# Performance work log

Measured on AMD Instinct MI355X. Metric: run time of the kernel, lower is better.

Reference implementation:

```python
import jax, jax.numpy as jnp
import numpy as np

INPUT_SIZE = 512
HIDDEN_SIZE = 512


def setup_inputs() -> dict:
    key = jax.random.key(0)
    k1, k2, k3, k4, k5 = jax.random.split(key, 5)
    B, N = 8, 2048
    x = jax.random.normal(k1, (B, N, INPUT_SIZE), dtype=jnp.float32)
    # Linear params (torch nn.Linear: y = x @ W^T + b), init scale ~ 1/sqrt(fan_in)
    s = 1.0 / np.sqrt(INPUT_SIZE)
    Wq = jax.random.uniform(k2, (HIDDEN_SIZE, INPUT_SIZE), minval=-s, maxval=s, dtype=jnp.float32)
    bq = jax.random.uniform(k3, (HIDDEN_SIZE,), minval=-s, maxval=s, dtype=jnp.float32)
    Wk = jax.random.uniform(k4, (HIDDEN_SIZE, INPUT_SIZE), minval=-s, maxval=s, dtype=jnp.float32)
    bk = jax.random.uniform(k5, (HIDDEN_SIZE,), minval=-s, maxval=s, dtype=jnp.float32)
    return {"x": x, "Wq": Wq, "bq": bq, "Wk": Wk, "bk": bk}


def reference(x, Wq, bq, Wk, bk):
    # q, k: [B, N, H]
    q = jnp.einsum('bnd,hd->bnh', x, Wq) + bq
    k = jnp.einsum('bnd,hd->bnh', x, Wk) + bk
    # scores: [B, N, N], softmax over last axis (dim=2)
    scores = jnp.einsum('bnh,bmh->bnm', q, k) / jnp.sqrt(jnp.float32(HIDDEN_SIZE))
    attn = jax.nn.softmax(scores, axis=2)
    # attended = attn^T @ x : [B, N, input_size]; squeeze(2) no-op since input_size>1
    attended = jnp.einsum('bnm,bnd->bmd', attn, x)
    return attended
```

## Files before the change

kernel.cpp:

```cpp
#include <hip/hip_runtime.h>

typedef __bf16 bf16x8 __attribute__((ext_vector_type(8)));
typedef float f32x4 __attribute__((ext_vector_type(4)));

__device__ __forceinline__ ushort f2bf(float f) {
    union { float f; unsigned u; } v; v.f = f;
    unsigned r = v.u + 0x7FFF + ((v.u >> 16) & 1);
    return (ushort)(r >> 16);
}

__device__ __forceinline__ void async_copy16(const void* g, void* l) {
    __builtin_amdgcn_global_load_lds(
        (const __attribute__((address_space(1))) void*)g,
        (__attribute__((address_space(3))) void*)l, 16, 0, 0);
}

__global__ __launch_bounds__(256) void cvt_kernel(
    const float4* __restrict__ x, const float4* __restrict__ Wq,
    const float4* __restrict__ Wk, const float4* __restrict__ bq,
    const float4* __restrict__ bk,
    ushort4* __restrict__ xb, ushort4* __restrict__ Wb,
    float4* __restrict__ biasc) {
    int i = blockIdx.x * 256 + threadIdx.x;
    if (i < 2097152) {
        float4 v = x[i];
        ushort4 r; r.x = f2bf(v.x); r.y = f2bf(v.y); r.z = f2bf(v.z); r.w = f2bf(v.w);
        xb[i] = r;
    }
    if (i < 131072) {
        float4 v = (i < 65536) ? Wq[i] : Wk[i - 65536];
        ushort4 r; r.x = f2bf(v.x); r.y = f2bf(v.y); r.z = f2bf(v.z); r.w = f2bf(v.w);
        Wb[i] = r;
    }
    if (i < 256) {
        biasc[i] = (i < 128) ? bq[i] : bk[i - 128];
    }
}

__global__ __launch_bounds__(256) void fold_kernel(
    const float* __restrict__ x, const float* __restrict__ Z,
    ushort* __restrict__ xzT) {
    __shared__ float tile[64][65];
    __shared__ float zin[64];
    const int b = blockIdx.y;
    const int td = blockIdx.x & 7;
    const int tn = blockIdx.x >> 3;
    const int n0 = tn * 64, d0 = td * 64;
    const int t = threadIdx.x;
    if (t < 64) zin[t] = 1.0f / Z[b * 2048 + n0 + t];
    __syncthreads();
    const int c = t & 63, r0 = t >> 6;
#pragma unroll
    for (int j = 0; j < 16; ++j) {
        int r = r0 + j * 4;
        tile[r][c] = x[((size_t)b * 2048 + n0 + r) * 512 + d0 + c] * zin[r];
    }
    __syncthreads();
#pragma unroll
    for (int j = 0; j < 16; ++j) {
        int dr = r0 + j * 4;
        xzT[((size_t)b * 512 + d0 + dr) * 2048 + n0 + c] = f2bf(tile[c][dr]);
    }
}

template <int EPI>
__global__ __launch_bounds__(256) void gemm_bt(
    const ushort* __restrict__ A, int lda, long sA,
    const ushort* __restrict__ B, int ldb, long sB,
    void* __restrict__ C, int ldc, long sC,
    int M, int N, int K,
    const float* __restrict__ bias, float scale,
    float* __restrict__ Z, long sZ) {
    __shared__ ushort lA[128 * 64];
    __shared__ ushort lB[128 * 64];
    const int b = blockIdx.y;
    A += (size_t)b * sA;
    B += (size_t)b * sB;
    const int tiles_n = N >> 7;
    const int tm = blockIdx.x / tiles_n, tn = blockIdx.x % tiles_n;
    const int t = threadIdx.x;
    const int l = t & 63, w = t >> 6;
    const int wr = w >> 1, wc = w & 1;

    f32x4 acc[4][4];
#pragma unroll
    for (int i = 0; i < 4; ++i)
#pragma unroll
        for (int j = 0; j < 4; ++j) acc[i][j] = (f32x4){0.f, 0.f, 0.f, 0.f};

    for (int k0 = 0; k0 < K; k0 += 64) {
#pragma unroll
        for (int p = 0; p < 4; ++p) {
            int off = p * 4096 + t * 16;
            int row = off >> 7;
            int kb = off & 127;
            int kswz = kb ^ ((row & 7) << 4);
            const ushort* srcA = A + (size_t)(tm * 128 + row) * lda + k0 + (kswz >> 1);
            async_copy16(srcA, (char*)lA + off);
            const ushort* srcB = B + (size_t)(tn * 128 + row) * ldb + k0 + (kswz >> 1);
            async_copy16(srcB, (char*)lB + off);
        }
        __syncthreads();
#pragma unroll
        for (int ks = 0; ks < 2; ++ks) {
            bf16x8 af[4], bfr[4];
#pragma unroll
            for (int i = 0; i < 4; ++i) {
                int row = wr * 64 + i * 16 + (l & 15);
                int colb = (ks * 64 + (l >> 4) * 16) ^ ((row & 7) << 4);
                af[i] = *(const bf16x8*)((const char*)lA + row * 128 + colb);
            }
#pragma unroll
            for (int j = 0; j < 4; ++j) {
                int row = wc * 64 + j * 16 + (l & 15);
                int colb = (ks * 64 + (l >> 4) * 16) ^ ((row & 7) << 4);
                bfr[j] = *(const bf16x8*)((const char*)lB + row * 128 + colb);
            }
#pragma unroll
            for (int i = 0; i < 4; ++i)
#pragma unroll
                for (int j = 0; j < 4; ++j)
                    acc[i][j] = __builtin_amdgcn_mfma_f32_16x16x32_bf16(
                        af[i], bfr[j], acc[i][j], 0, 0, 0);
        }
        __syncthreads();
    }

    const int m_base = tm * 128 + wr * 64;
    const int n_base = tn * 128 + wc * 64;

    if (EPI == 0) {
        ushort* Cp = (ushort*)C + (size_t)b * sC;
#pragma unroll
        for (int i = 0; i < 4; ++i)
#pragma unroll
            for (int j = 0; j < 4; ++j)
#pragma unroll
                for (int q = 0; q < 4; ++q) {
                    int row = m_base + i * 16 + (l >> 4) * 4 + q;
                    int col = n_base + j * 16 + (l & 15);
                    Cp[(size_t)row * ldc + col] = f2bf(acc[i][j][q] + bias[col]);
                }
    } else if (EPI == 1) {
        ushort* Cp = (ushort*)C + (size_t)b * sC;
        float colsum[4] = {0.f, 0.f, 0.f, 0.f};
#pragma unroll
        for (int i = 0; i < 4; ++i)
#pragma unroll
            for (int j = 0; j < 4; ++j)
#pragma unroll
                for (int q = 0; q < 4; ++q) {
                    int row = m_base + i * 16 + (l >> 4) * 4 + q;
                    int col = n_base + j * 16 + (l & 15);
                    float e = __expf(acc[i][j][q] * scale);
                    Cp[(size_t)row * ldc + col] = f2bf(e);
                    colsum[j] += e;
                }
#pragma unroll
        for (int j = 0; j < 4; ++j) {
            float s = colsum[j];
            s += __shfl_xor(s, 16);
            s += __shfl_xor(s, 32);
            if (l < 16) atomicAdd(&Z[b * sZ + n_base + j * 16 + l], s);
        }
    } else {
        float* Cp = (float*)C + (size_t)b * sC;
#pragma unroll
        for (int i = 0; i < 4; ++i)
#pragma unroll
            for (int j = 0; j < 4; ++j)
#pragma unroll
                for (int q = 0; q < 4; ++q) {
                    int row = m_base + i * 16 + (l >> 4) * 4 + q;
                    int col = n_base + j * 16 + (l & 15);
                    Cp[(size_t)row * ldc + col] = acc[i][j][q];
                }
    }
}

extern "C" void kernel_launch(void* const* d_in, const int* in_sizes, int n_in,
                              void* d_out, int out_size, void* d_ws, size_t ws_size,
                              hipStream_t stream) {
    const float* x  = (const float*)d_in[0];
    const float* Wq = (const float*)d_in[1];
    const float* bq = (const float*)d_in[2];
    const float* Wk = (const float*)d_in[3];
    const float* bk = (const float*)d_in[4];

    char* ws = (char*)d_ws;
    ushort* xb    = (ushort*)(ws);
    ushort* Wb    = (ushort*)(ws + 16777216);
    float*  biasc = (float*) (ws + 17825792);
    float*  Z     = (float*) (ws + 17829888);
    ushort* qkb   = (ushort*)(ws + 17895424);
    ushort* E     = (ushort*)(ws + 51449856);
    ushort* xzT   = xb;

    hipMemsetAsync(Z, 0, 16384 * 4, stream);

    cvt_kernel<<<8192, 256, 0, stream>>>(
        (const float4*)x, (const float4*)Wq, (const float4*)Wk,
        (const float4*)bq, (const float4*)bk,
        (ushort4*)xb, (ushort4*)Wb, (float4*)biasc);

    gemm_bt<0><<<dim3(1024, 1), 256, 0, stream>>>(
        xb, 512, 0L, Wb, 512, 0L, qkb, 1024, 0L,
        16384, 1024, 512, biasc, 0.f, nullptr, 0L);

    gemm_bt<1><<<dim3(256, 8), 256, 0, stream>>>(
        qkb + 512, 1024, 2048L * 1024, qkb, 1024, 2048L * 1024,
        E, 2048, 2048L * 2048, 2048, 2048, 512,
        nullptr, 0.04419417382415922f, Z, 2048L);

    fold_kernel<<<dim3(256, 8), 256, 0, stream>>>(x, Z, xzT);

    gemm_bt<2><<<dim3(64, 8), 256, 0, stream>>>(
        E, 2048, 2048L * 2048, xzT, 2048, 512L * 2048,
        d_out, 512, 2048L * 512, 2048, 512, 2048,
        nullptr, 0.f, nullptr, 0L);
}
```

Baseline: 154.4 us.

## Vectorize bf16 epilogue stores with column permutation and fold from bf16 input

The GEMM epilogues now pack four accumulator columns into one 8-byte bf16 store instead of scattered 2-byte stores. This permutes columns within each 64-wide block, and the code keeps that consistent: the Z atomics, the fold kernel's normalizer indexing and the q/k hidden dimension all follow the same permutation. The fold kernel reads the bf16 copy of x with vector loads instead of the fp32 original and writes packed bf16x4, which cuts its memory traffic. Manual rounding is replaced by native __bf16 conversions. The permuted layout is subtle and fragile, but the indexing appears consistent.

```diff
diff --git a/kernel.cpp b/kernel.cpp
--- a/kernel.cpp
+++ b/kernel.cpp
@@ -1,13 +1,8 @@
 #include <hip/hip_runtime.h>
 
 typedef __bf16 bf16x8 __attribute__((ext_vector_type(8)));
+typedef __bf16 bf16x4 __attribute__((ext_vector_type(4)));
 typedef float f32x4 __attribute__((ext_vector_type(4)));
-
-__device__ __forceinline__ ushort f2bf(float f) {
-    union { float f; unsigned u; } v; v.f = f;
-    unsigned r = v.u + 0x7FFF + ((v.u >> 16) & 1);
-    return (ushort)(r >> 16);
-}
 
 __device__ __forceinline__ void async_copy16(const void* g, void* l) {
     __builtin_amdgcn_global_load_lds(
@@ -19,17 +14,17 @@
     const float4* __restrict__ x, const float4* __restrict__ Wq,
     const float4* __restrict__ Wk, const float4* __restrict__ bq,
     const float4* __restrict__ bk,
-    ushort4* __restrict__ xb, ushort4* __restrict__ Wb,
+    bf16x4* __restrict__ xb, bf16x4* __restrict__ Wb,
     float4* __restrict__ biasc) {
     int i = blockIdx.x * 256 + threadIdx.x;
     if (i < 2097152) {
         float4 v = x[i];
-        ushort4 r; r.x = f2bf(v.x); r.y = f2bf(v.y); r.z = f2bf(v.z); r.w = f2bf(v.w);
+        bf16x4 r = {(__bf16)v.x, (__bf16)v.y, (__bf16)v.z, (__bf16)v.w};
         xb[i] = r;
     }
     if (i < 131072) {
         float4 v = (i < 65536) ? Wq[i] : Wk[i - 65536];
-        ushort4 r; r.x = f2bf(v.x); r.y = f2bf(v.y); r.z = f2bf(v.z); r.w = f2bf(v.w);
+        bf16x4 r = {(__bf16)v.x, (__bf16)v.y, (__bf16)v.z, (__bf16)v.w};
         Wb[i] = r;
     }
     if (i < 256) {
@@ -38,7 +33,7 @@
 }
 
 __global__ __launch_bounds__(256) void fold_kernel(
-    const float* __restrict__ x, const float* __restrict__ Z,
+    const __bf16* __restrict__ xb, const float* __restrict__ Z,
     ushort* __restrict__ xzT) {
     __shared__ float tile[64][65];
     __shared__ float zin[64];
@@ -49,17 +44,25 @@
     const int t = threadIdx.x;
     if (t < 64) zin[t] = 1.0f / Z[b * 2048 + n0 + t];
     __syncthreads();
-    const int c = t & 63, r0 = t >> 6;
-#pragma unroll
-    for (int j = 0; j < 16; ++j) {
-        int r = r0 + j * 4;
-        tile[r][c] = x[((size_t)b * 2048 + n0 + r) * 512 + d0 + c] * zin[r];
+    const int cl = t & 15, c4 = cl * 4, rr = t >> 4;
+#pragma unroll
+    for (int j = 0; j < 4; ++j) {
+        int nr = rr + j * 16;
+        bf16x4 v = *(const bf16x4*)&xb[((size_t)b * 2048 + n0 + nr) * 512 + d0 + c4];
+        tile[nr][c4 + 0] = (float)v[0];
+        tile[nr][c4 + 1] = (float)v[1];
+        tile[nr][c4 + 2] = (float)v[2];
+        tile[nr][c4 + 3] = (float)v[3];
     }
     __syncthreads();
 #pragma unroll
-    for (int j = 0; j < 16; ++j) {
-        int dr = r0 + j * 4;
-        xzT[((size_t)b * 512 + d0 + dr) * 2048 + n0 + c] = f2bf(tile[c][dr]);
+    for (int j2 = 0; j2 < 4; ++j2) {
+        int dr = rr + j2 * 16;
+        bf16x4 pk;
+#pragma unroll
+        for (int j = 0; j < 4; ++j)
+            pk[j] = (__bf16)(tile[j * 16 + cl][dr] * zin[c4 + j]);
+        *(bf16x4*)&xzT[((size_t)b * 512 + d0 + dr) * 2048 + n0 + c4] = pk;
     }
 }
 
@@ -68,7 +71,7 @@
     const ushort* __restrict__ A, int lda, long sA,
     const ushort* __restrict__ B, int ldb, long sB,
     void* __restrict__ C, int ldc, long sC,
-    int M, int N, int K,
+    int tiles_n, int K,
     const float* __restrict__ bias, float scale,
     float* __restrict__ Z, long sZ) {
     __shared__ ushort lA[128 * 64];
@@ -76,7 +79,6 @@
     const int b = blockIdx.y;
     A += (size_t)b * sA;
     B += (size_t)b * sB;
-    const int tiles_n = N >> 7;
     const int tm = blockIdx.x / tiles_n, tn = blockIdx.x % tiles_n;
     const int t = threadIdx.x;
     const int l = t & 63, w = t >> 6;
@@ -95,10 +97,10 @@
             int row = off >> 7;
             int kb = off & 127;
             int kswz = kb ^ ((row & 7) << 4);
-            const ushort* srcA = A + (size_t)(tm * 128 + row) * lda + k0 + (kswz >> 1);
-            async_copy16(srcA, (char*)lA + off);
-            const ushort* srcB = B + (size_t)(tn * 128 + row) * ldb + k0 + (kswz >> 1);
-            async_copy16(srcB, (char*)lB + off);
+            async_copy16(A + (size_t)(tm * 128 + row) * lda + k0 + (kswz >> 1),
+                         (char*)lA + off);
+            async_copy16(B + (size_t)(tn * 128 + row) * ldb + k0 + (kswz >> 1),
+                         (char*)lB + off);
         }
         __syncthreads();
 #pragma unroll
@@ -126,42 +128,46 @@
         __syncthreads();
     }
 
-    const int m_base = tm * 128 + wr * 64;
-    const int n_base = tn * 128 + wc * 64;
+    const int mb = tm * 128 + wr * 64;
+    const int nb = tn * 128 + wc * 64;
+    const int cl = l & 15;
 
     if (EPI == 0) {
         ushort* Cp = (ushort*)C + (size_t)b * sC;
 #pragma unroll
         for (int i = 0; i < 4; ++i)
 #pragma unroll
-            for (int j = 0; j < 4; ++j)
-#pragma unroll
-                for (int q = 0; q < 4; ++q) {
-                    int row = m_base + i * 16 + (l >> 4) * 4 + q;
-                    int col = n_base + j * 16 + (l & 15);
-                    Cp[(size_t)row * ldc + col] = f2bf(acc[i][j][q] + bias[col]);
-                }
+            for (int q = 0; q < 4; ++q) {
+                int row = mb + i * 16 + (l >> 4) * 4 + q;
+                bf16x4 pk;
+#pragma unroll
+                for (int j = 0; j < 4; ++j)
+                    pk[j] = (__bf16)(acc[i][j][q] + bias[nb + j * 16 + cl]);
+                *(bf16x4*)&Cp[(size_t)row * ldc + nb + cl * 4] = pk;
+            }
     } else if (EPI == 1) {
         ushort* Cp = (ushort*)C + (size_t)b * sC;
         float colsum[4] = {0.f, 0.f, 0.f, 0.f};
 #pragma unroll
         for (int i = 0; i < 4; ++i)
 #pragma unroll
-            for (int j = 0; j < 4; ++j)
-#pragma unroll
-                for (int q = 0; q < 4; ++q) {
-                    int row = m_base + i * 16 + (l >> 4) * 4 + q;
-                    int col = n_base + j * 16 + (l & 15);
+            for (int q = 0; q < 4; ++q) {
+                int row = mb + i * 16 + (l >> 4) * 4 + q;
+                bf16x4 pk;
+#pragma unroll
+                for (int j = 0; j < 4; ++j) {
                     float e = __expf(acc[i][j][q] * scale);
-                    Cp[(size_t)row * ldc + col] = f2bf(e);
                     colsum[j] += e;
+                    pk[j] = (__bf16)e;
                 }
+                *(bf16x4*)&Cp[(size_t)row * ldc + nb + cl * 4] = pk;
+            }
 #pragma unroll
         for (int j = 0; j < 4; ++j) {
             float s = colsum[j];
             s += __shfl_xor(s, 16);
             s += __shfl_xor(s, 32);
-            if (l < 16) atomicAdd(&Z[b * sZ + n_base + j * 16 + l], s);
+            if (l < 16) atomicAdd(&Z[b * sZ + nb + l * 4 + j], s);
         }
     } else {
         float* Cp = (float*)C + (size_t)b * sC;
@@ -171,8 +177,8 @@
             for (int j = 0; j < 4; ++j)
 #pragma unroll
                 for (int q = 0; q < 4; ++q) {
-                    int row = m_base + i * 16 + (l >> 4) * 4 + q;
-                    int col = n_base + j * 16 + (l & 15);
+                    int row = mb + i * 16 + (l >> 4) * 4 + q;
+                    int col = nb + j * 16 + cl;
                     Cp[(size_t)row * ldc + col] = acc[i][j][q];
                 }
     }
@@ -194,28 +200,28 @@
     float*  Z     = (float*) (ws + 17829888);
     ushort* qkb   = (ushort*)(ws + 17895424);
     ushort* E     = (ushort*)(ws + 51449856);
-    ushort* xzT   = xb;
+    ushort* xzT   = qkb;
 
     hipMemsetAsync(Z, 0, 16384 * 4, stream);
 
     cvt_kernel<<<8192, 256, 0, stream>>>(
         (const float4*)x, (const float4*)Wq, (const float4*)Wk,
         (const float4*)bq, (const float4*)bk,
-        (ushort4*)xb, (ushort4*)Wb, (float4*)biasc);
+        (bf16x4*)xb, (bf16x4*)Wb, (float4*)biasc);
 
     gemm_bt<0><<<dim3(1024, 1), 256, 0, stream>>>(
         xb, 512, 0L, Wb, 512, 0L, qkb, 1024, 0L,
-        16384, 1024, 512, biasc, 0.f, nullptr, 0L);
+        8, 512, biasc, 0.f, nullptr, 0L);
 
     gemm_bt<1><<<dim3(256, 8), 256, 0, stream>>>(
         qkb + 512, 1024, 2048L * 1024, qkb, 1024, 2048L * 1024,
-        E, 2048, 2048L * 2048, 2048, 2048, 512,
+        E, 2048, 2048L * 2048, 16, 512,
         nullptr, 0.04419417382415922f, Z, 2048L);
 
-    fold_kernel<<<dim3(256, 8), 256, 0, stream>>>(x, Z, xzT);
+    fold_kernel<<<dim3(256, 8), 256, 0, stream>>>((const __bf16*)xb, Z, xzT);
 
     gemm_bt<2><<<dim3(64, 8), 256, 0, stream>>>(
         E, 2048, 2048L * 2048, xzT, 2048, 512L * 2048,
-        d_out, 512, 2048L * 512, 2048, 512, 2048,
+        d_out, 512, 2048L * 512, 4, 2048,
         nullptr, 0.f, nullptr, 0L);
 }
```

New measurement: 154.8 us. Within noise of the previous version (+0.3%).
